# Kernel optimization log

Measured on AMD Instinct MI355X. Metric: run time of the kernel, lower is better.

Reference implementation:

```python
import jax, jax.numpy as jnp
import numpy as np

TSZ, BSZ, E, H = 1024, 8, 1024, 16


def setup_inputs() -> dict:
    key = jax.random.key(0)
    ks = jax.random.split(key, 7)
    s = 0.02
    return {
        "q": jax.random.normal(ks[0], (TSZ, BSZ, E), jnp.float32),
        "k": jax.random.normal(ks[1], (TSZ, BSZ, E), jnp.float32),
        "v": jax.random.normal(ks[2], (TSZ, BSZ, E), jnp.float32),
        "in_proj_weight": jax.random.normal(ks[3], (3 * E, E), jnp.float32) * s,
        "in_proj_bias": jax.random.normal(ks[4], (3 * E,), jnp.float32) * s,
        "out_proj_weight": jax.random.normal(ks[5], (E, E), jnp.float32) * s,
        "out_proj_bias": jax.random.normal(ks[6], (E,), jnp.float32) * s,
        "num_heads": H,
    }


def reference(q, k, v, in_proj_weight, in_proj_bias, out_proj_weight, out_proj_bias, num_heads):
    tsz, bsz, embed_dim = q.shape
    head_dim = embed_dim // num_heads
    scaling = float(head_dim) ** -0.5

    # in-projections (F.linear: x @ W.T + b), weight sliced into q/k/v chunks
    qp = q @ in_proj_weight[:embed_dim].T + in_proj_bias[:embed_dim]
    kp = k @ in_proj_weight[embed_dim:2 * embed_dim].T + in_proj_bias[embed_dim:2 * embed_dim]
    vp = v @ in_proj_weight[2 * embed_dim:].T + in_proj_bias[2 * embed_dim:]
    qp = qp * scaling

    # (tsz, bsz, E) -> (bsz*H, tsz, head_dim)
    def to_heads(x):
        return x.reshape(tsz, bsz * num_heads, head_dim).transpose(1, 0, 2)

    qh, kh, vh = to_heads(qp), to_heads(kp), to_heads(vp)

    # scaled dot-product attention (no mask, dropout p=0)
    scores = jnp.einsum('bqd,bkd->bqk', qh, kh)  # [bsz*H, tsz, tsz]
    weights = jax.nn.softmax(scores, axis=-1)
    attn = jnp.einsum('bqk,bkd->bqd', weights, vh)

    # back to (tsz, bsz, E), then out projection
    attn = attn.transpose(1, 0, 2).reshape(tsz, bsz, embed_dim)
    out = attn @ out_proj_weight.T + out_proj_bias
    return out
```

## Files before the change

### kernel.cpp

```cpp
#include <hip/hip_runtime.h>

typedef __bf16 bf16;
typedef __attribute__((ext_vector_type(8))) __bf16 v8bf;
typedef __attribute__((ext_vector_type(4))) __bf16 v4bf;
typedef __attribute__((ext_vector_type(4))) float f32x4;

static_assert(sizeof(v8bf) == 16, "v8bf must be 16B");

#define MFMA16(a, b, c) __builtin_amdgcn_mfma_f32_16x16x32_bf16((a), (b), (c), 0, 0, 0)

__device__ __forceinline__ void async_lds16(const bf16* g, bf16* l) {
  __builtin_amdgcn_global_load_lds(
      (__attribute__((address_space(1))) void*)(g),
      (__attribute__((address_space(3))) void*)(l), 16, 0, 0);
}

__global__ __launch_bounds__(256) void cvt_kernel(
    const float* __restrict__ q, const float* __restrict__ k,
    const float* __restrict__ v, const float* __restrict__ wi,
    const float* __restrict__ wo, bf16* __restrict__ xq, bf16* __restrict__ xk,
    bf16* __restrict__ xv, bf16* __restrict__ Wb, bf16* __restrict__ Wob) {
  int idx = blockIdx.x * 256 + threadIdx.x;
  const float4* src;
  v4bf* dst;
  int off;
  if (idx < 2097152)      { src = (const float4*)q;  dst = (v4bf*)xq;  off = idx; }
  else if (idx < 4194304) { src = (const float4*)k;  dst = (v4bf*)xk;  off = idx - 2097152; }
  else if (idx < 6291456) { src = (const float4*)v;  dst = (v4bf*)xv;  off = idx - 4194304; }
  else if (idx < 7077888) { src = (const float4*)wi; dst = (v4bf*)Wb;  off = idx - 6291456; }
  else                    { src = (const float4*)wo; dst = (v4bf*)Wob; off = idx - 7077888; }
  float4 f = src[off];
  v4bf b;
  b[0] = (bf16)f.x; b[1] = (bf16)f.y; b[2] = (bf16)f.z; b[3] = (bf16)f.w;
  dst[off] = b;
}

#define STAGE_A(S, MH, KO)                                                    \
  do {                                                                        \
    async_lds16(Xa + (size_t)((MH) * 128 + srA0) * 1024 + (KO) + skA0,        \
                &Asm[S][MH][ldst]);                                           \
    async_lds16(Xa + (size_t)((MH) * 128 + srA1) * 1024 + (KO) + skA1,        \
                &Asm[S][MH][4096 + ldst]);                                    \
  } while (0)

#define STAGE_B(S, NH, KO)                                                    \
  async_lds16(Wbase + (size_t)((NH) * 64 + srB) * 1024 + (KO) + skB,          \
              &Bsm[S][NH][ldst])

#define KTILE(S, NS, KN)                                                      \
  do {                                                                        \
    v8bf af0[4][2], af1[4][2], bf0[2], bf1[2];                                \
                                                            \
    _Pragma("unroll") for (int rt = 0; rt < 4; ++rt) {                        \
      af0[rt][0] = *(const v8bf*)&Asm[S][0][aro + rt * 1024 + rslot0];        \
      af0[rt][1] = *(const v8bf*)&Asm[S][0][aro + rt * 1024 + rslot1];        \
    }                                                                         \
    bf0[0] = *(const v8bf*)&Bsm[S][0][bro + rslot0];                          \
    bf0[1] = *(const v8bf*)&Bsm[S][0][bro + rslot1];                          \
    STAGE_A(NS, 0, KN);                                                       \
    asm volatile("s_waitcnt vmcnt(2)" ::: "memory");                          \
    __builtin_amdgcn_s_barrier();                                             \
    __builtin_amdgcn_s_setprio(1);                                            \
    _Pragma("unroll") for (int rt = 0; rt < 4; ++rt) {                        \
      acc[rt][0] = MFMA16(af0[rt][0], bf0[0], acc[rt][0]);                    \
      acc[rt][0] = MFMA16(af0[rt][1], bf0[1], acc[rt][0]);                    \
    }                                                                         \
    __builtin_amdgcn_s_setprio(0);                                            \
                                                            \
    _Pragma("unroll") for (int rt = 0; rt < 4; ++rt) {                        \
      af1[rt][0] = *(const v8bf*)&Asm[S][1][aro + rt * 1024 + rslot0];        \
      af1[rt][1] = *(const v8bf*)&Asm[S][1][aro + rt * 1024 + rslot1];        \
    }                                                                         \
    bf1[0] = *(const v8bf*)&Bsm[S][1][bro + rslot0];                          \
    bf1[1] = *(const v8bf*)&Bsm[S][1][bro + rslot1];                          \
    STAGE_B(NS, 0, KN);                                                       \
    __builtin_amdgcn_s_barrier();                                             \
    __builtin_amdgcn_s_setprio(1);                                            \
    _Pragma("unroll") for (int rt = 0; rt < 4; ++rt) {                        \
      acc[4 + rt][1] = MFMA16(af1[rt][0], bf1[0], acc[4 + rt][1]);            \
      acc[4 + rt][1] = MFMA16(af1[rt][1], bf1[1], acc[4 + rt][1]);            \
    }                                                                         \
    __builtin_amdgcn_s_setprio(0);                                            \
                                                            \
    STAGE_A(NS, 1, KN);                                                       \
    __builtin_amdgcn_s_barrier();                                             \
    __builtin_amdgcn_s_setprio(1);                                            \
    _Pragma("unroll") for (int rt = 0; rt < 4; ++rt) {                        \
      acc[4 + rt][0] = MFMA16(af1[rt][0], bf0[0], acc[4 + rt][0]);            \
      acc[4 + rt][0] = MFMA16(af1[rt][1], bf0[1], acc[4 + rt][0]);            \
    }                                                                         \
    __builtin_amdgcn_s_setprio(0);                                            \
                                                            \
    STAGE_B(NS, 1, KN);                                                       \
    asm volatile("s_waitcnt vmcnt(3)" ::: "memory");                          \
    __builtin_amdgcn_s_barrier();                                             \
    __builtin_amdgcn_s_setprio(1);                                            \
    _Pragma("unroll") for (int rt = 0; rt < 4; ++rt) {                        \
      acc[rt][1] = MFMA16(af0[rt][0], bf1[0], acc[rt][1]);                    \
      acc[rt][1] = MFMA16(af0[rt][1], bf1[1], acc[rt][1]);                    \
    }                                                                         \
    __builtin_amdgcn_s_setprio(0);                                            \
  } while (0)

#define GEMM_PRELUDE()                                                        \
  const int tid = threadIdx.x;                                                \
  const int w = tid >> 6, l = tid & 63, quad = l >> 4, lr = l & 15;           \
  const int wmg = w >> 2, wng = w & 3;                                        \
  const int srA0 = tid >> 3;                                                  \
  const int skA0 = (((tid & 7) ^ (srA0 & 7)) * 8);                            \
  const int srA1 = (512 + tid) >> 3;                                          \
  const int skA1 = (((tid & 7) ^ (srA1 & 7)) * 8);                            \
  const int srB = tid >> 3;                                                   \
  const int skB = (((tid & 7) ^ (srB & 7)) * 8);                              \
  const int ldst = (tid & ~63) * 8;                                           \
  const int aro = (wmg * 64 + lr) * 64;                                       \
  const int bro = (wng * 16 + lr) * 64;                                       \
  const int rslot0 = ((quad) ^ (lr & 7)) * 8;                                 \
  const int rslot1 = ((4 + quad) ^ (lr & 7)) * 8;                             \
  f32x4 acc[8][2] = {};                                                       \
        \
  STAGE_A(0, 0, 0);                                                           \
  STAGE_B(0, 0, 0);                                                           \
  STAGE_A(0, 1, 0);                                                           \
  STAGE_B(0, 1, 0);                                                           \
  asm volatile("s_waitcnt vmcnt(3)" ::: "memory");                            \
  __builtin_amdgcn_s_barrier();                                               \
  _Pragma("unroll 1") for (int t = 0; t < 16; t += 2) {                       \
    const int k1 = (t + 1) * 64;                                              \
    const int k2 = (t == 14) ? 0 : (t + 2) * 64;  \
    KTILE(0, 1, k1);                                                          \
    KTILE(1, 0, k2);                                                          \
  }                                                                           \
  asm volatile("s_waitcnt vmcnt(0)" ::: "memory");

__global__ __launch_bounds__(512, 2) void qkv_proj_kernel(
    const bf16* __restrict__ xq, const bf16* __restrict__ xk,
    const bf16* __restrict__ xv, const bf16* __restrict__ Wb,
    const float* __restrict__ bias, bf16* __restrict__ oq,
    bf16* __restrict__ ok, bf16* __restrict__ ov) {
  __shared__ bf16 Asm[2][2][128 * 64];
  __shared__ bf16 Bsm[2][2][64 * 64];
  const int L = blockIdx.x;
  const int r = L & 7, rest = L >> 3;
  const int m0 = (r * 4 + (rest & 3)) * 256;
  const int n0 = ((rest >> 2) & 7) * 128;
  const int c = rest >> 5;
  const bf16* X = (c == 0) ? xq : (c == 1) ? xk : xv;
  bf16* outp = (c == 0) ? oq : (c == 1) ? ok : ov;
  const bf16* Xa = X + (size_t)m0 * 1024;
  const bf16* Wbase = Wb + ((size_t)(c * 1024 + n0)) * 1024;

  GEMM_PRELUDE();

  const float scale = (c == 0) ? 0.125f : 1.0f;
#pragma unroll
  for (int mh = 0; mh < 2; ++mh)
#pragma unroll
    for (int rt = 0; rt < 4; ++rt)
#pragma unroll
      for (int nh = 0; nh < 2; ++nh) {
        const int n = n0 + nh * 64 + wng * 16 + lr;
        const float bn = bias[c * 1024 + n];
        const int hh = n >> 6, d = n & 63;
#pragma unroll
        for (int j = 0; j < 4; ++j) {
          const int m = m0 + mh * 128 + wmg * 64 + rt * 16 + quad * 4 + j;
          const int t_ = m >> 3, b = m & 7;
          outp[((size_t)((b * 16 + hh) * 1024 + t_)) * 64 + d] =
              (bf16)((acc[mh * 4 + rt][nh][j] + bn) * scale);
        }
      }
}

__global__ __launch_bounds__(256) void transpose_v_kernel(const bf16* __restrict__ vin,
                                                          bf16* __restrict__ vout) {
  __shared__ bf16 tile[64][72];
  const int bh = blockIdx.x;
  const int t0 = blockIdx.y * 64;
  const int tid = threadIdx.x;
  const int row = tid >> 2, cg = (tid & 3) * 16;
  const bf16* src = vin + ((size_t)bh * 1024 + t0 + row) * 64 + cg;
#pragma unroll
  for (int i = 0; i < 2; ++i) {
    v8bf x = *(const v8bf*)(src + i * 8);
#pragma unroll
    for (int jj = 0; jj < 8; ++jj) tile[row][cg + i * 8 + jj] = x[jj];
  }
  __syncthreads();
  const int d = tid >> 2, tg = (tid & 3) * 16;
  bf16* dst = vout + ((size_t)bh * 64 + d) * 1024 + t0 + tg;
  v8bf o0, o1;
#pragma unroll
  for (int i = 0; i < 8; ++i) o0[i] = tile[tg + i][d];
#pragma unroll
  for (int i = 0; i < 8; ++i) o1[i] = tile[tg + 8 + i][d];
  *(v8bf*)dst = o0;
  *(v8bf*)(dst + 8) = o1;
}

#define KSTR 72
#define VSTR 136

__global__ __launch_bounds__(256, 2) void attn_kernel(const bf16* __restrict__ qh,
                                                      const bf16* __restrict__ kh,
                                                      const bf16* __restrict__ vT,
                                                      bf16* __restrict__ attn_out) {
  __shared__ bf16 Ksm[128 * KSTR];
  __shared__ bf16 Vsm[64 * VSTR];
  __shared__ bf16 Psm[128 * VSTR];
  const int L = blockIdx.x;
  const int bh = (L & 7) * 16 + ((L >> 3) & 15);
  const int t0 = (L >> 7) * 128;
  const int tid = threadIdx.x;
  const int w = tid >> 6, l = tid & 63, quad = l >> 4, lr = l & 15;
  const int qr0 = t0 + w * 32;

  const bf16* khead = kh + (size_t)bh * 1024 * 64;
  const bf16* vhead = vT + (size_t)bh * 64 * 1024;

  const size_t qbase = ((size_t)bh * 1024 + qr0 + lr) * 64 + quad * 8;
  const v8bf bq00 = *(const v8bf*)(qh + qbase);
  const v8bf bq01 = *(const v8bf*)(qh + qbase + 32);
  const v8bf bq10 = *(const v8bf*)(qh + qbase + 1024);
  const v8bf bq11 = *(const v8bf*)(qh + qbase + 1024 + 32);

  const int krow = tid >> 1, kd = (tid & 1) * 32;
  const int vrow = tid >> 2, vk = (tid & 3) * 32;
  const bf16* kg = khead + (size_t)krow * 64 + kd;
  const bf16* vg = vhead + (size_t)vrow * 1024 + vk;
  bf16* Kw = &Ksm[krow * KSTR + kd];
  bf16* Vw = &Vsm[vrow * VSTR + vk];
  bf16* Pw = &Psm[w * 32 * VSTR];

  v8bf kst[4], vst[4];
#pragma unroll
  for (int i = 0; i < 4; ++i) kst[i] = *(const v8bf*)(kg + i * 8);
#pragma unroll
  for (int i = 0; i < 4; ++i) vst[i] = *(const v8bf*)(vg + i * 8);

  float rsum0 = 0.0f, rsum1 = 0.0f;
  f32x4 oacc0[4] = {}, oacc1[4] = {};

  for (int c = 0; c < 8; ++c) {
    __syncthreads();
#pragma unroll
    for (int i = 0; i < 4; ++i) *(v8bf*)(Kw + i * 8) = kst[i];
#pragma unroll
    for (int i = 0; i < 4; ++i) *(v8bf*)(Vw + i * 8) = vst[i];
    __syncthreads();
    if (c < 7) {
      const bf16* kg2 = kg + (size_t)(c + 1) * 128 * 64;
      const bf16* vg2 = vg + (c + 1) * 128;
#pragma unroll
      for (int i = 0; i < 4; ++i) kst[i] = *(const v8bf*)(kg2 + i * 8);
#pragma unroll
      for (int i = 0; i < 4; ++i) vst[i] = *(const v8bf*)(vg2 + i * 8);
    }

#pragma unroll
    for (int kt = 0; kt < 8; ++kt) {
      const v8bf ak0 = *(const v8bf*)&Ksm[(kt * 16 + lr) * KSTR + quad * 8];
      const v8bf ak1 = *(const v8bf*)&Ksm[(kt * 16 + lr) * KSTR + 32 + quad * 8];
      f32x4 a = {};
      a = MFMA16(ak0, bq00, a);
      a = MFMA16(ak1, bq01, a);
      f32x4 b = {};
      b = MFMA16(ak0, bq10, b);
      b = MFMA16(ak1, bq11, b);
      v4bf pb0, pb1;
#pragma unroll
      for (int j = 0; j < 4; ++j) {
        const float p0 = __expf(a[j]);
        const float p1 = __expf(b[j]);
        rsum0 += p0;
        rsum1 += p1;
        pb0[j] = (bf16)p0;
        pb1[j] = (bf16)p1;
      }
      *(v4bf*)(Pw + lr * VSTR + kt * 16 + quad * 4) = pb0;
      *(v4bf*)(Pw + (16 + lr) * VSTR + kt * 16 + quad * 4) = pb1;
    }

#pragma unroll
    for (int ks = 0; ks < 4; ++ks) {
      const v8bf pa0 = *(const v8bf*)(Pw + lr * VSTR + ks * 32 + quad * 8);
      const v8bf pa1 = *(const v8bf*)(Pw + (16 + lr) * VSTR + ks * 32 + quad * 8);
#pragma unroll
      for (int dt = 0; dt < 4; ++dt) {
        const v8bf vb = *(const v8bf*)&Vsm[(dt * 16 + lr) * VSTR + ks * 32 + quad * 8];
        oacc0[dt] = MFMA16(pa0, vb, oacc0[dt]);
        oacc1[dt] = MFMA16(pa1, vb, oacc1[dt]);
      }
    }
  }

  rsum0 += __shfl_xor(rsum0, 16);
  rsum0 += __shfl_xor(rsum0, 32);
  rsum1 += __shfl_xor(rsum1, 16);
  rsum1 += __shfl_xor(rsum1, 32);
  const float inv0 = 1.0f / rsum0;
  const float inv1 = 1.0f / rsum1;
  const int b = bh >> 4, h = bh & 15;
#pragma unroll
  for (int j = 0; j < 4; ++j) {
    const float i0 = __shfl(inv0, quad * 4 + j);
    const float i1 = __shfl(inv1, quad * 4 + j);
    const int t0j = qr0 + quad * 4 + j;
#pragma unroll
    for (int dt = 0; dt < 4; ++dt) {
      attn_out[((size_t)(t0j * 8 + b)) * 1024 + h * 64 + dt * 16 + lr] =
          (bf16)(oacc0[dt][j] * i0);
      attn_out[((size_t)((t0j + 16) * 8 + b)) * 1024 + h * 64 + dt * 16 + lr] =
          (bf16)(oacc1[dt][j] * i1);
    }
  }
}

__global__ __launch_bounds__(512, 2) void out_proj_kernel(const bf16* __restrict__ A,
                                                          const bf16* __restrict__ Wob,
                                                          const float* __restrict__ bias,
                                                          float* __restrict__ out) {
  __shared__ bf16 Asm[2][2][128 * 64];
  __shared__ bf16 Bsm[2][2][64 * 64];
  const int L = blockIdx.x;
  const int r = L & 7, rest = L >> 3;
  const int m0 = (r * 4 + (rest & 3)) * 256;
  const int n0 = (rest >> 2) * 128;
  const bf16* Xa = A + (size_t)m0 * 1024;
  const bf16* Wbase = Wob + (size_t)n0 * 1024;

  GEMM_PRELUDE();

#pragma unroll
  for (int mh = 0; mh < 2; ++mh)
#pragma unroll
    for (int rt = 0; rt < 4; ++rt)
#pragma unroll
      for (int nh = 0; nh < 2; ++nh) {
        const int n = n0 + nh * 64 + wng * 16 + lr;
        const float bn = bias[n];
#pragma unroll
        for (int j = 0; j < 4; ++j) {
          const int m = m0 + mh * 128 + wmg * 64 + rt * 16 + quad * 4 + j;
          out[(size_t)m * 1024 + n] = acc[mh * 4 + rt][nh][j] + bn;
        }
      }
}

extern "C" void kernel_launch(void* const* d_in, const int* in_sizes, int n_in,
                              void* d_out, int out_size, void* d_ws, size_t ws_size,
                              hipStream_t stream) {
  const float* q  = (const float*)d_in[0];
  const float* k  = (const float*)d_in[1];
  const float* v  = (const float*)d_in[2];
  const float* wi = (const float*)d_in[3];
  const float* bi = (const float*)d_in[4];
  const float* wo = (const float*)d_in[5];
  const float* bo = (const float*)d_in[6];
  float* out = (float*)d_out;
  char* ws = (char*)d_ws;
  const size_t MB = (size_t)1 << 20;
  bf16* Wb     = (bf16*)(ws + 0 * MB);
  bf16* Wob    = (bf16*)(ws + 6 * MB);
  bf16* wsq    = (bf16*)(ws + 8 * MB);
  bf16* wsk    = (bf16*)(ws + 24 * MB);
  bf16* wsv    = (bf16*)(ws + 40 * MB);
  bf16* xv     = (bf16*)(ws + 56 * MB);
  bf16* wsvT   = (bf16*)(ws + 56 * MB);
  bf16* xq     = (bf16*)d_out;
  bf16* xk     = (bf16*)((char*)d_out + 16 * MB);
  bf16* wsattn = wsv;

  cvt_kernel<<<dim3(28672), dim3(256), 0, stream>>>(q, k, v, wi, wo, xq, xk, xv, Wb, Wob);
  qkv_proj_kernel<<<dim3(768), dim3(512), 0, stream>>>(xq, xk, xv, Wb, bi, wsq, wsk, wsv);
  transpose_v_kernel<<<dim3(128, 16), dim3(256), 0, stream>>>(wsv, wsvT);
  attn_kernel<<<dim3(1024), dim3(256), 0, stream>>>(wsq, wsk, wsvT, wsattn);
  out_proj_kernel<<<dim3(512 / 2), dim3(512), 0, stream>>>(wsattn, Wob, bo, out);
}
```

Measured before the change: 296.3 us.

## Triple-buffer GEMM K-tiles and remap warps to 64x64 output subtiles

The shared GEMM prelude used by the QKV and output projections moves from a double-buffered split half-tile pipeline to a three-stage ring of full 256x64 A and 128x64 B tiles, prefetching two K-tiles ahead. Each of the 8 warps now owns a 64x64 output block (4x4 MFMA tiles) instead of 128x32, which lets A and B fragments be reused across more MFMAs per LDS read. The aim is to hide global-load latency better and cut LDS traffic per MFMA. In exchange, LDS use rises to 144KB per block, which could limit occupancy to one block per CU despite launch bounds requesting two.

```diff
diff --git a/kernel.cpp b/kernel.cpp
--- a/kernel.cpp
+++ b/kernel.cpp
@@ -35,69 +35,72 @@
   dst[off] = b;
 }
 
-#define STAGE_A(S, MH, KO)                                                    \
+#define A_TSZ (256 * 64)
+#define B_TSZ (128 * 64)
+
+#define STAGE6(SBUF, KO)                                                      \
   do {                                                                        \
-    async_lds16(Xa + (size_t)((MH) * 128 + srA0) * 1024 + (KO) + skA0,        \
-                &Asm[S][MH][ldst]);                                           \
-    async_lds16(Xa + (size_t)((MH) * 128 + srA1) * 1024 + (KO) + skA1,        \
-                &Asm[S][MH][4096 + ldst]);                                    \
+    bf16* Ad = Asmb + (SBUF) * A_TSZ + ldst;                                  \
+    bf16* Bd = Bsmb + (SBUF) * B_TSZ + ldst;                                  \
+    _Pragma("unroll") for (int i = 0; i < 4; ++i)                             \
+        async_lds16(Xa + (size_t)sAr[i] * 1024 + (KO) + sAk[i],               \
+                    Ad + i * 4096);                                           \
+    _Pragma("unroll") for (int i = 0; i < 2; ++i)                             \
+        async_lds16(Wbase + (size_t)sBr[i] * 1024 + (KO) + sBk[i],            \
+                    Bd + i * 4096);                                           \
   } while (0)
 
-#define STAGE_B(S, NH, KO)                                                    \
-  async_lds16(Wbase + (size_t)((NH) * 64 + srB) * 1024 + (KO) + skB,          \
-              &Bsm[S][NH][ldst])
-
-#define KTILE(S, NS, KN)                                                      \
+#define KTILE_BODY(CUR, STAGE_STMT, WAIT_STMT)                                \
   do {                                                                        \
-    v8bf af0[4][2], af1[4][2], bf0[2], bf1[2];                                \
-                                                            \
-    _Pragma("unroll") for (int rt = 0; rt < 4; ++rt) {                        \
-      af0[rt][0] = *(const v8bf*)&Asm[S][0][aro + rt * 1024 + rslot0];        \
-      af0[rt][1] = *(const v8bf*)&Asm[S][0][aro + rt * 1024 + rslot1];        \
-    }                                                                         \
-    bf0[0] = *(const v8bf*)&Bsm[S][0][bro + rslot0];                          \
-    bf0[1] = *(const v8bf*)&Bsm[S][0][bro + rslot1];                          \
-    STAGE_A(NS, 0, KN);                                                       \
-    asm volatile("s_waitcnt vmcnt(2)" ::: "memory");                          \
+    const bf16* Ab = Asmb + (CUR) * A_TSZ;                                    \
+    const bf16* Bb = Bsmb + (CUR) * B_TSZ;                                    \
+    v8bf af0[4], af1[4], bf0[4], bf1[4];                                      \
+                                      \
+    _Pragma("unroll") for (int rt = 0; rt < 4; ++rt)                          \
+        af0[rt] = *(const v8bf*)&Ab[aro + rt * 1024 + rslot0];                \
+    bf0[0] = *(const v8bf*)&Bb[bro + rslot0];                                 \
+    bf0[1] = *(const v8bf*)&Bb[bro + 1024 + rslot0];                          \
     __builtin_amdgcn_s_barrier();                                             \
     __builtin_amdgcn_s_setprio(1);                                            \
     _Pragma("unroll") for (int rt = 0; rt < 4; ++rt) {                        \
-      acc[rt][0] = MFMA16(af0[rt][0], bf0[0], acc[rt][0]);                    \
-      acc[rt][0] = MFMA16(af0[rt][1], bf0[1], acc[rt][0]);                    \
+      acc[rt][0] = MFMA16(af0[rt], bf0[0], acc[rt][0]);                       \
+      acc[rt][1] = MFMA16(af0[rt], bf0[1], acc[rt][1]);                       \
     }                                                                         \
     __builtin_amdgcn_s_setprio(0);                                            \
-                                                            \
-    _Pragma("unroll") for (int rt = 0; rt < 4; ++rt) {                        \
-      af1[rt][0] = *(const v8bf*)&Asm[S][1][aro + rt * 1024 + rslot0];        \
-      af1[rt][1] = *(const v8bf*)&Asm[S][1][aro + rt * 1024 + rslot1];        \
-    }                                                                         \
-    bf1[0] = *(const v8bf*)&Bsm[S][1][bro + rslot0];                          \
-    bf1[1] = *(const v8bf*)&Bsm[S][1][bro + rslot1];                          \
-    STAGE_B(NS, 0, KN);                                                       \
+                           \
+    bf0[2] = *(const v8bf*)&Bb[bro + 2048 + rslot0];                          \
+    bf0[3] = *(const v8bf*)&Bb[bro + 3072 + rslot0];                          \
+    af1[0] = *(const v8bf*)&Ab[aro + rslot1];                                 \
+    af1[1] = *(const v8bf*)&Ab[aro + 1024 + rslot1];                          \
+    STAGE_STMT                                                                \
     __builtin_amdgcn_s_barrier();                                             \
     __builtin_amdgcn_s_setprio(1);                                            \
     _Pragma("unroll") for (int rt = 0; rt < 4; ++rt) {                        \
-      acc[4 + rt][1] = MFMA16(af1[rt][0], bf1[0], acc[4 + rt][1]);            \
-      acc[4 + rt][1] = MFMA16(af1[rt][1], bf1[1], acc[4 + rt][1]);            \
+      acc[rt][2] = MFMA16(af0[rt], bf0[2], acc[rt][2]);                       \
+      acc[rt][3] = MFMA16(af0[rt], bf0[3], acc[rt][3]);                       \
     }                                                                         \
     __builtin_amdgcn_s_setprio(0);                                            \
-                                                            \
-    STAGE_A(NS, 1, KN);                                                       \
+                                      \
+    af1[2] = *(const v8bf*)&Ab[aro + 2048 + rslot1];                          \
+    af1[3] = *(const v8bf*)&Ab[aro + 3072 + rslot1];                          \
+    bf1[0] = *(const v8bf*)&Bb[bro + rslot1];                                 \
+    bf1[1] = *(const v8bf*)&Bb[bro + 1024 + rslot1];                          \
     __builtin_amdgcn_s_barrier();                                             \
     __builtin_amdgcn_s_setprio(1);                                            \
     _Pragma("unroll") for (int rt = 0; rt < 4; ++rt) {                        \
-      acc[4 + rt][0] = MFMA16(af1[rt][0], bf0[0], acc[4 + rt][0]);            \
-      acc[4 + rt][0] = MFMA16(af1[rt][1], bf0[1], acc[4 + rt][0]);            \
+      acc[rt][0] = MFMA16(af1[rt], bf1[0], acc[rt][0]);                       \
+      acc[rt][1] = MFMA16(af1[rt], bf1[1], acc[rt][1]);                       \
     }                                                                         \
     __builtin_amdgcn_s_setprio(0);                                            \
-                                                            \
-    STAGE_B(NS, 1, KN);                                                       \
-    asm volatile("s_waitcnt vmcnt(3)" ::: "memory");                          \
+                                          \
+    bf1[2] = *(const v8bf*)&Bb[bro + 2048 + rslot1];                          \
+    bf1[3] = *(const v8bf*)&Bb[bro + 3072 + rslot1];                          \
+    WAIT_STMT                                                                 \
     __builtin_amdgcn_s_barrier();                                             \
     __builtin_amdgcn_s_setprio(1);                                            \
     _Pragma("unroll") for (int rt = 0; rt < 4; ++rt) {                        \
-      acc[rt][1] = MFMA16(af0[rt][0], bf1[0], acc[rt][1]);                    \
-      acc[rt][1] = MFMA16(af0[rt][1], bf1[1], acc[rt][1]);                    \
+      acc[rt][2] = MFMA16(af1[rt], bf1[2], acc[rt][2]);                       \
+      acc[rt][3] = MFMA16(af1[rt], bf1[3], acc[rt][3]);                       \
     }                                                                         \
     __builtin_amdgcn_s_setprio(0);                                            \
   } while (0)
@@ -105,41 +108,50 @@
 #define GEMM_PRELUDE()                                                        \
   const int tid = threadIdx.x;                                                \
   const int w = tid >> 6, l = tid & 63, quad = l >> 4, lr = l & 15;           \
-  const int wmg = w >> 2, wng = w & 3;                                        \
-  const int srA0 = tid >> 3;                                                  \
-  const int skA0 = (((tid & 7) ^ (srA0 & 7)) * 8);                            \
-  const int srA1 = (512 + tid) >> 3;                                          \
-  const int skA1 = (((tid & 7) ^ (srA1 & 7)) * 8);                            \
-  const int srB = tid >> 3;                                                   \
-  const int skB = (((tid & 7) ^ (srB & 7)) * 8);                              \
+  const int wmg = w >> 1, wng = w & 1;                                        \
+  int sAr[4], sAk[4];                                                         \
+  _Pragma("unroll") for (int i = 0; i < 4; ++i) {                             \
+    sAr[i] = (i * 512 + tid) >> 3;                                            \
+    sAk[i] = ((tid & 7) ^ (sAr[i] & 7)) * 8;                                  \
+  }                                                                           \
+  int sBr[2], sBk[2];                                                         \
+  _Pragma("unroll") for (int i = 0; i < 2; ++i) {                             \
+    sBr[i] = (i * 512 + tid) >> 3;                                            \
+    sBk[i] = ((tid & 7) ^ (sBr[i] & 7)) * 8;                                  \
+  }                                                                           \
   const int ldst = (tid & ~63) * 8;                                           \
   const int aro = (wmg * 64 + lr) * 64;                                       \
-  const int bro = (wng * 16 + lr) * 64;                                       \
+  const int bro = (wng * 64 + lr) * 64;                                       \
   const int rslot0 = ((quad) ^ (lr & 7)) * 8;                                 \
   const int rslot1 = ((4 + quad) ^ (lr & 7)) * 8;                             \
-  f32x4 acc[8][2] = {};                                                       \
-        \
-  STAGE_A(0, 0, 0);                                                           \
-  STAGE_B(0, 0, 0);                                                           \
-  STAGE_A(0, 1, 0);                                                           \
-  STAGE_B(0, 1, 0);                                                           \
-  asm volatile("s_waitcnt vmcnt(3)" ::: "memory");                            \
+  f32x4 acc[4][4] = {};                                                       \
+       \
+  STAGE6(0, 0);                                                               \
+  STAGE6(1, 64);                                                              \
+  asm volatile("s_waitcnt vmcnt(6)" ::: "memory");                            \
   __builtin_amdgcn_s_barrier();                                               \
-  _Pragma("unroll 1") for (int t = 0; t < 16; t += 2) {                       \
-    const int k1 = (t + 1) * 64;                                              \
-    const int k2 = (t == 14) ? 0 : (t + 2) * 64;  \
-    KTILE(0, 1, k1);                                                          \
-    KTILE(1, 0, k2);                                                          \
+  int cur = 0;                                                                \
+  _Pragma("unroll 1") for (int t = 0; t < 14; ++t) {                          \
+    const int nxt = (cur >= 1) ? cur - 1 : 2;                  \
+    KTILE_BODY(cur, STAGE6(nxt, (t + 2) * 64);,                               \
+               asm volatile("s_waitcnt vmcnt(6)" ::: "memory"););             \
+    cur = (cur == 2) ? 0 : cur + 1;                                           \
   }                                                                           \
-  asm volatile("s_waitcnt vmcnt(0)" ::: "memory");
+            \
+  KTILE_BODY(cur, , asm volatile("s_waitcnt vmcnt(0)" ::: "memory"););        \
+  cur = (cur == 2) ? 0 : cur + 1;                                             \
+                                               \
+  KTILE_BODY(cur, , )
 
 __global__ __launch_bounds__(512, 2) void qkv_proj_kernel(
     const bf16* __restrict__ xq, const bf16* __restrict__ xk,
     const bf16* __restrict__ xv, const bf16* __restrict__ Wb,
     const float* __restrict__ bias, bf16* __restrict__ oq,
     bf16* __restrict__ ok, bf16* __restrict__ ov) {
-  __shared__ bf16 Asm[2][2][128 * 64];
-  __shared__ bf16 Bsm[2][2][64 * 64];
+  __shared__ bf16 Asm[3][A_TSZ];
+  __shared__ bf16 Bsm[3][B_TSZ];
+  bf16* Asmb = &Asm[0][0];
+  bf16* Bsmb = &Bsm[0][0];
   const int L = blockIdx.x;
   const int r = L & 7, rest = L >> 3;
   const int m0 = (r * 4 + (rest & 3)) * 256;
@@ -154,22 +166,20 @@
 
   const float scale = (c == 0) ? 0.125f : 1.0f;
 #pragma unroll
-  for (int mh = 0; mh < 2; ++mh)
-#pragma unroll
-    for (int rt = 0; rt < 4; ++rt)
-#pragma unroll
-      for (int nh = 0; nh < 2; ++nh) {
-        const int n = n0 + nh * 64 + wng * 16 + lr;
-        const float bn = bias[c * 1024 + n];
-        const int hh = n >> 6, d = n & 63;
-#pragma unroll
-        for (int j = 0; j < 4; ++j) {
-          const int m = m0 + mh * 128 + wmg * 64 + rt * 16 + quad * 4 + j;
-          const int t_ = m >> 3, b = m & 7;
-          outp[((size_t)((b * 16 + hh) * 1024 + t_)) * 64 + d] =
-              (bf16)((acc[mh * 4 + rt][nh][j] + bn) * scale);
-        }
+  for (int rt = 0; rt < 4; ++rt)
+#pragma unroll
+    for (int ct = 0; ct < 4; ++ct) {
+      const int n = n0 + wng * 64 + ct * 16 + lr;
+      const float bn = bias[c * 1024 + n];
+      const int hh = n >> 6, d = n & 63;
+#pragma unroll
+      for (int j = 0; j < 4; ++j) {
+        const int m = m0 + wmg * 64 + rt * 16 + quad * 4 + j;
+        const int t_ = m >> 3, b = m & 7;
+        outp[((size_t)((b * 16 + hh) * 1024 + t_)) * 64 + d] =
+            (bf16)((acc[rt][ct][j] + bn) * scale);
       }
+    }
 }
 
 __global__ __launch_bounds__(256) void transpose_v_kernel(const bf16* __restrict__ vin,
@@ -320,8 +330,10 @@
                                                           const bf16* __restrict__ Wob,
                                                           const float* __restrict__ bias,
                                                           float* __restrict__ out) {
-  __shared__ bf16 Asm[2][2][128 * 64];
-  __shared__ bf16 Bsm[2][2][64 * 64];
+  __shared__ bf16 Asm[3][A_TSZ];
+  __shared__ bf16 Bsm[3][B_TSZ];
+  bf16* Asmb = &Asm[0][0];
+  bf16* Bsmb = &Bsm[0][0];
   const int L = blockIdx.x;
   const int r = L & 7, rest = L >> 3;
   const int m0 = (r * 4 + (rest & 3)) * 256;
@@ -332,19 +344,17 @@
   GEMM_PRELUDE();
 
 #pragma unroll
-  for (int mh = 0; mh < 2; ++mh)
-#pragma unroll
-    for (int rt = 0; rt < 4; ++rt)
-#pragma unroll
-      for (int nh = 0; nh < 2; ++nh) {
-        const int n = n0 + nh * 64 + wng * 16 + lr;
-        const float bn = bias[n];
-#pragma unroll
-        for (int j = 0; j < 4; ++j) {
-          const int m = m0 + mh * 128 + wmg * 64 + rt * 16 + quad * 4 + j;
-          out[(size_t)m * 1024 + n] = acc[mh * 4 + rt][nh][j] + bn;
-        }
+  for (int rt = 0; rt < 4; ++rt)
+#pragma unroll
+    for (int ct = 0; ct < 4; ++ct) {
+      const int n = n0 + wng * 64 + ct * 16 + lr;
+      const float bn = bias[n];
+#pragma unroll
+      for (int j = 0; j < 4; ++j) {
+        const int m = m0 + wmg * 64 + rt * 16 + quad * 4 + j;
+        out[(size_t)m * 1024 + n] = acc[rt][ct][j] + bn;
       }
+    }
 }
 
 extern "C" void kernel_launch(void* const* d_in, const int* in_sizes, int n_in,
@@ -375,5 +385,5 @@
   qkv_proj_kernel<<<dim3(768), dim3(512), 0, stream>>>(xq, xk, xv, Wb, bi, wsq, wsk, wsv);
   transpose_v_kernel<<<dim3(128, 16), dim3(256), 0, stream>>>(wsv, wsvT);
   attn_kernel<<<dim3(1024), dim3(256), 0, stream>>>(wsq, wsk, wsvT, wsattn);
-  out_proj_kernel<<<dim3(512 / 2), dim3(512), 0, stream>>>(wsattn, Wob, bo, out);
-}
+  out_proj_kernel<<<dim3(256), dim3(512), 0, stream>>>(wsattn, Wob, bo, out);
+}
```

After: 300.8 us. No clear change (+1.5%).

## Rewrite projection GEMMs with 256x256 tiles and 32x32x16 MFMA

Applied to the files above, without the earlier changes.

Replaces the 256x128 tile, 512-thread GEMM core used by the QKV and output projections with a 256x256 tile, 256-thread design. Each wave computes a 128x128 sub-tile using 32x32x16 bf16 MFMAs, with a new XOR swizzle and simple double buffering. Larger per-wave tiles raise register reuse and cut LDS reads per FLOP. In exchange, the grids shrink to 384 and 128 blocks at one block per CU, so occupancy and the number of blocks per CU drop. The previous fine-grained interleaving of staging and compute is gone, replaced by a full vmcnt(0) wait per tile.

```diff
diff --git a/kernel.cpp b/kernel.cpp
--- a/kernel.cpp
+++ b/kernel.cpp
@@ -4,10 +4,12 @@
 typedef __attribute__((ext_vector_type(8))) __bf16 v8bf;
 typedef __attribute__((ext_vector_type(4))) __bf16 v4bf;
 typedef __attribute__((ext_vector_type(4))) float f32x4;
+typedef __attribute__((ext_vector_type(16))) float f32x16;
 
 static_assert(sizeof(v8bf) == 16, "v8bf must be 16B");
 
 #define MFMA16(a, b, c) __builtin_amdgcn_mfma_f32_16x16x32_bf16((a), (b), (c), 0, 0, 0)
+#define MFMA32(a, b, c) __builtin_amdgcn_mfma_f32_32x32x16_bf16((a), (b), (c), 0, 0, 0)
 
 __device__ __forceinline__ void async_lds16(const bf16* g, bf16* l) {
   __builtin_amdgcn_global_load_lds(
@@ -35,141 +37,123 @@
   dst[off] = b;
 }
 
-#define STAGE_A(S, MH, KO)                                                    \
+#define TSZ (256 * 64)
+
+#define STAGE32(BUF, KO)                                                      \
   do {                                                                        \
-    async_lds16(Xa + (size_t)((MH) * 128 + srA0) * 1024 + (KO) + skA0,        \
-                &Asm[S][MH][ldst]);                                           \
-    async_lds16(Xa + (size_t)((MH) * 128 + srA1) * 1024 + (KO) + skA1,        \
-                &Asm[S][MH][4096 + ldst]);                                    \
+    bf16* Ad = Asmb + (BUF) * TSZ + wdst;                                     \
+    bf16* Bd = Bsmb + (BUF) * TSZ + wdst;                                     \
+    _Pragma("unroll") for (int i = 0; i < 8; ++i)                             \
+        async_lds16(Xa + (size_t)sOff[i] + (KO), Ad + i * 2048);              \
+    _Pragma("unroll") for (int i = 0; i < 8; ++i)                             \
+        async_lds16(Wbase + (size_t)sOff[i] + (KO), Bd + i * 2048);           \
   } while (0)
 
-#define STAGE_B(S, NH, KO)                                                    \
-  async_lds16(Wbase + (size_t)((NH) * 64 + srB) * 1024 + (KO) + skB,          \
-              &Bsm[S][NH][ldst])
-
-#define KTILE(S, NS, KN)                                                      \
+#define LOADA(BUF, MH)                                                        \
+  _Pragma("unroll") for (int ks = 0; ks < 4; ++ks) {                          \
+    aR[0][ks] = *(const v8bf*)&Asmb[(BUF) * TSZ + aBase + (MH) * 4096 +       \
+                                    ((ks * 16) ^ plA8)];                      \
+    aR[1][ks] = *(const v8bf*)&Asmb[(BUF) * TSZ + aBase + (MH) * 4096 +       \
+                                    2048 + ((ks * 16) ^ 32 ^ plA8)];          \
+  }
+
+#define LOADB(BUF, NH)                                                        \
+  _Pragma("unroll") for (int ks = 0; ks < 4; ++ks) {                          \
+    bR[NH][0][ks] = *(const v8bf*)&Bsmb[(BUF) * TSZ + bBase + (NH) * 4096 +   \
+                                        ((ks * 16) ^ plA8)];                  \
+    bR[NH][1][ks] = *(const v8bf*)&Bsmb[(BUF) * TSZ + bBase + (NH) * 4096 +   \
+                                        2048 + ((ks * 16) ^ 32 ^ plA8)];      \
+  }
+
+#define MFMAQ(MH, NH)                                                         \
+  _Pragma("unroll") for (int ks = 0; ks < 4; ++ks) {                          \
+    acc[(MH)*2+0][(NH)*2+0] =                                                 \
+        MFMA32(aR[0][ks], bR[NH][0][ks], acc[(MH)*2+0][(NH)*2+0]);            \
+    acc[(MH)*2+0][(NH)*2+1] =                                                 \
+        MFMA32(aR[0][ks], bR[NH][1][ks], acc[(MH)*2+0][(NH)*2+1]);            \
+    acc[(MH)*2+1][(NH)*2+0] =                                                 \
+        MFMA32(aR[1][ks], bR[NH][0][ks], acc[(MH)*2+1][(NH)*2+0]);            \
+    acc[(MH)*2+1][(NH)*2+1] =                                                 \
+        MFMA32(aR[1][ks], bR[NH][1][ks], acc[(MH)*2+1][(NH)*2+1]);            \
+  }
+
+#define TILE32(BUF, STAGE_STMT)                                               \
   do {                                                                        \
-    v8bf af0[4][2], af1[4][2], bf0[2], bf1[2];                                \
-                                                            \
-    _Pragma("unroll") for (int rt = 0; rt < 4; ++rt) {                        \
-      af0[rt][0] = *(const v8bf*)&Asm[S][0][aro + rt * 1024 + rslot0];        \
-      af0[rt][1] = *(const v8bf*)&Asm[S][0][aro + rt * 1024 + rslot1];        \
-    }                                                                         \
-    bf0[0] = *(const v8bf*)&Bsm[S][0][bro + rslot0];                          \
-    bf0[1] = *(const v8bf*)&Bsm[S][0][bro + rslot1];                          \
-    STAGE_A(NS, 0, KN);                                                       \
-    asm volatile("s_waitcnt vmcnt(2)" ::: "memory");                          \
+    STAGE_STMT;                                                               \
+    LOADA(BUF, 0)                                                             \
+    LOADB(BUF, 0)                                                             \
+    MFMAQ(0, 0)                                                               \
+    LOADB(BUF, 1)                                                             \
+    MFMAQ(0, 1)                                                               \
+    LOADA(BUF, 1)                                                             \
+    MFMAQ(1, 1)                                                               \
+    MFMAQ(1, 0)                                                               \
+    asm volatile("s_waitcnt vmcnt(0)" ::: "memory");                          \
     __builtin_amdgcn_s_barrier();                                             \
-    __builtin_amdgcn_s_setprio(1);                                            \
-    _Pragma("unroll") for (int rt = 0; rt < 4; ++rt) {                        \
-      acc[rt][0] = MFMA16(af0[rt][0], bf0[0], acc[rt][0]);                    \
-      acc[rt][0] = MFMA16(af0[rt][1], bf0[1], acc[rt][0]);                    \
-    }                                                                         \
-    __builtin_amdgcn_s_setprio(0);                                            \
-                                                            \
-    _Pragma("unroll") for (int rt = 0; rt < 4; ++rt) {                        \
-      af1[rt][0] = *(const v8bf*)&Asm[S][1][aro + rt * 1024 + rslot0];        \
-      af1[rt][1] = *(const v8bf*)&Asm[S][1][aro + rt * 1024 + rslot1];        \
-    }                                                                         \
-    bf1[0] = *(const v8bf*)&Bsm[S][1][bro + rslot0];                          \
-    bf1[1] = *(const v8bf*)&Bsm[S][1][bro + rslot1];                          \
-    STAGE_B(NS, 0, KN);                                                       \
-    __builtin_amdgcn_s_barrier();                                             \
-    __builtin_amdgcn_s_setprio(1);                                            \
-    _Pragma("unroll") for (int rt = 0; rt < 4; ++rt) {                        \
-      acc[4 + rt][1] = MFMA16(af1[rt][0], bf1[0], acc[4 + rt][1]);            \
-      acc[4 + rt][1] = MFMA16(af1[rt][1], bf1[1], acc[4 + rt][1]);            \
-    }                                                                         \
-    __builtin_amdgcn_s_setprio(0);                                            \
-                                                            \
-    STAGE_A(NS, 1, KN);                                                       \
-    __builtin_amdgcn_s_barrier();                                             \
-    __builtin_amdgcn_s_setprio(1);                                            \
-    _Pragma("unroll") for (int rt = 0; rt < 4; ++rt) {                        \
-      acc[4 + rt][0] = MFMA16(af1[rt][0], bf0[0], acc[4 + rt][0]);            \
-      acc[4 + rt][0] = MFMA16(af1[rt][1], bf0[1], acc[4 + rt][0]);            \
-    }                                                                         \
-    __builtin_amdgcn_s_setprio(0);                                            \
-                                                            \
-    STAGE_B(NS, 1, KN);                                                       \
-    asm volatile("s_waitcnt vmcnt(3)" ::: "memory");                          \
-    __builtin_amdgcn_s_barrier();                                             \
-    __builtin_amdgcn_s_setprio(1);                                            \
-    _Pragma("unroll") for (int rt = 0; rt < 4; ++rt) {                        \
-      acc[rt][1] = MFMA16(af0[rt][0], bf1[0], acc[rt][1]);                    \
-      acc[rt][1] = MFMA16(af0[rt][1], bf1[1], acc[rt][1]);                    \
-    }                                                                         \
-    __builtin_amdgcn_s_setprio(0);                                            \
   } while (0)
 
-#define GEMM_PRELUDE()                                                        \
+#define GEMM32_PRELUDE()                                                      \
   const int tid = threadIdx.x;                                                \
-  const int w = tid >> 6, l = tid & 63, quad = l >> 4, lr = l & 15;           \
-  const int wmg = w >> 2, wng = w & 3;                                        \
-  const int srA0 = tid >> 3;                                                  \
-  const int skA0 = (((tid & 7) ^ (srA0 & 7)) * 8);                            \
-  const int srA1 = (512 + tid) >> 3;                                          \
-  const int skA1 = (((tid & 7) ^ (srA1 & 7)) * 8);                            \
-  const int srB = tid >> 3;                                                   \
-  const int skB = (((tid & 7) ^ (srB & 7)) * 8);                              \
-  const int ldst = (tid & ~63) * 8;                                           \
-  const int aro = (wmg * 64 + lr) * 64;                                       \
-  const int bro = (wng * 16 + lr) * 64;                                       \
-  const int rslot0 = ((quad) ^ (lr & 7)) * 8;                                 \
-  const int rslot1 = ((4 + quad) ^ (lr & 7)) * 8;                             \
-  f32x4 acc[8][2] = {};                                                       \
-        \
-  STAGE_A(0, 0, 0);                                                           \
-  STAGE_B(0, 0, 0);                                                           \
-  STAGE_A(0, 1, 0);                                                           \
-  STAGE_B(0, 1, 0);                                                           \
-  asm volatile("s_waitcnt vmcnt(3)" ::: "memory");                            \
+  const int w = tid >> 6, l = tid & 63;                                       \
+  const int wm = w >> 1, wn = w & 1;                                          \
+  const int c31 = l & 31, kh = l >> 5;                                        \
+  const int plA8 = ((kh ^ c31 ^ (c31 >> 3)) & 7) * 8;                         \
+  const int aBase = (wm * 128 + c31) * 64;                                    \
+  const int bBase = (wn * 128 + c31) * 64;                                    \
+  const int wdst = (tid & ~63) * 8;                                           \
+  int sOff[8];                                                                \
+  _Pragma("unroll") for (int i = 0; i < 8; ++i) {                             \
+    const int ch = i * 256 + tid;                                             \
+    const int rw = ch >> 3;                                                   \
+    sOff[i] = rw * 1024 + (((ch & 7) ^ ((rw ^ (rw >> 3)) & 7)) * 8);          \
+  }                                                                           \
+  v8bf aR[2][4], bR[2][2][4];                                                 \
+  f32x16 acc[4][4] = {};                                                      \
+  STAGE32(0, 0);                                                              \
+  asm volatile("s_waitcnt vmcnt(0)" ::: "memory");                            \
   __builtin_amdgcn_s_barrier();                                               \
   _Pragma("unroll 1") for (int t = 0; t < 16; t += 2) {                       \
-    const int k1 = (t + 1) * 64;                                              \
-    const int k2 = (t == 14) ? 0 : (t + 2) * 64;  \
-    KTILE(0, 1, k1);                                                          \
-    KTILE(1, 0, k2);                                                          \
-  }                                                                           \
-  asm volatile("s_waitcnt vmcnt(0)" ::: "memory");
-
-__global__ __launch_bounds__(512, 2) void qkv_proj_kernel(
+    TILE32(0, STAGE32(1, (t + 1) * 64));                                      \
+    TILE32(1, if (t < 14) STAGE32(0, (t + 2) * 64));                          \
+  }
+
+__global__ __launch_bounds__(256, 1) void qkv_proj_kernel(
     const bf16* __restrict__ xq, const bf16* __restrict__ xk,
     const bf16* __restrict__ xv, const bf16* __restrict__ Wb,
     const float* __restrict__ bias, bf16* __restrict__ oq,
     bf16* __restrict__ ok, bf16* __restrict__ ov) {
-  __shared__ bf16 Asm[2][2][128 * 64];
-  __shared__ bf16 Bsm[2][2][64 * 64];
+  __shared__ bf16 Asm2[2][TSZ];
+  __shared__ bf16 Bsm2[2][TSZ];
+  bf16* Asmb = &Asm2[0][0];
+  bf16* Bsmb = &Bsm2[0][0];
   const int L = blockIdx.x;
-  const int r = L & 7, rest = L >> 3;
-  const int m0 = (r * 4 + (rest & 3)) * 256;
-  const int n0 = ((rest >> 2) & 7) * 128;
-  const int c = rest >> 5;
+  const int g = L >> 5;
+  const int c = g >> 2;
+  const int n0 = (g & 3) * 256;
+  const int m0 = (L & 31) * 256;
   const bf16* X = (c == 0) ? xq : (c == 1) ? xk : xv;
   bf16* outp = (c == 0) ? oq : (c == 1) ? ok : ov;
   const bf16* Xa = X + (size_t)m0 * 1024;
   const bf16* Wbase = Wb + ((size_t)(c * 1024 + n0)) * 1024;
 
-  GEMM_PRELUDE();
+  GEMM32_PRELUDE();
 
   const float scale = (c == 0) ? 0.125f : 1.0f;
 #pragma unroll
-  for (int mh = 0; mh < 2; ++mh)
-#pragma unroll
-    for (int rt = 0; rt < 4; ++rt)
-#pragma unroll
-      for (int nh = 0; nh < 2; ++nh) {
-        const int n = n0 + nh * 64 + wng * 16 + lr;
-        const float bn = bias[c * 1024 + n];
-        const int hh = n >> 6, d = n & 63;
-#pragma unroll
-        for (int j = 0; j < 4; ++j) {
-          const int m = m0 + mh * 128 + wmg * 64 + rt * 16 + quad * 4 + j;
-          const int t_ = m >> 3, b = m & 7;
-          outp[((size_t)((b * 16 + hh) * 1024 + t_)) * 64 + d] =
-              (bf16)((acc[mh * 4 + rt][nh][j] + bn) * scale);
-        }
+  for (int mf = 0; mf < 4; ++mf)
+#pragma unroll
+    for (int nf = 0; nf < 4; ++nf) {
+      const int n = n0 + wn * 128 + nf * 32 + c31;
+      const float bn = bias[c * 1024 + n];
+      const int hh = n >> 6, d = n & 63;
+#pragma unroll
+      for (int r = 0; r < 16; ++r) {
+        const int m = m0 + wm * 128 + mf * 32 + (r & 3) + ((r >> 2) * 8) + kh * 4;
+        const int t_ = m >> 3, b = m & 7;
+        outp[((size_t)((b * 16 + hh) * 1024 + t_)) * 64 + d] =
+            (bf16)((acc[mf][nf][r] + bn) * scale);
       }
+    }
 }
 
 __global__ __launch_bounds__(256) void transpose_v_kernel(const bf16* __restrict__ vin,
@@ -316,35 +300,34 @@
   }
 }
 
-__global__ __launch_bounds__(512, 2) void out_proj_kernel(const bf16* __restrict__ A,
+__global__ __launch_bounds__(256, 1) void out_proj_kernel(const bf16* __restrict__ A,
                                                           const bf16* __restrict__ Wob,
                                                           const float* __restrict__ bias,
                                                           float* __restrict__ out) {
-  __shared__ bf16 Asm[2][2][128 * 64];
-  __shared__ bf16 Bsm[2][2][64 * 64];
+  __shared__ bf16 Asm2[2][TSZ];
+  __shared__ bf16 Bsm2[2][TSZ];
+  bf16* Asmb = &Asm2[0][0];
+  bf16* Bsmb = &Bsm2[0][0];
   const int L = blockIdx.x;
-  const int r = L & 7, rest = L >> 3;
-  const int m0 = (r * 4 + (rest & 3)) * 256;
-  const int n0 = (rest >> 2) * 128;
+  const int n0 = (L >> 5) * 256;
+  const int m0 = (L & 31) * 256;
   const bf16* Xa = A + (size_t)m0 * 1024;
   const bf16* Wbase = Wob + (size_t)n0 * 1024;
 
-  GEMM_PRELUDE();
-
-#pragma unroll
-  for (int mh = 0; mh < 2; ++mh)
-#pragma unroll
-    for (int rt = 0; rt < 4; ++rt)
-#pragma unroll
-      for (int nh = 0; nh < 2; ++nh) {
-        const int n = n0 + nh * 64 + wng * 16 + lr;
-        const float bn = bias[n];
-#pragma unroll
-        for (int j = 0; j < 4; ++j) {
-          const int m = m0 + mh * 128 + wmg * 64 + rt * 16 + quad * 4 + j;
-          out[(size_t)m * 1024 + n] = acc[mh * 4 + rt][nh][j] + bn;
-        }
+  GEMM32_PRELUDE();
+
+#pragma unroll
+  for (int mf = 0; mf < 4; ++mf)
+#pragma unroll
+    for (int nf = 0; nf < 4; ++nf) {
+      const int n = n0 + wn * 128 + nf * 32 + c31;
+      const float bn = bias[n];
+#pragma unroll
+      for (int r = 0; r < 16; ++r) {
+        const int m = m0 + wm * 128 + mf * 32 + (r & 3) + ((r >> 2) * 8) + kh * 4;
+        out[(size_t)m * 1024 + n] = acc[mf][nf][r] + bn;
       }
+    }
 }
 
 extern "C" void kernel_launch(void* const* d_in, const int* in_sizes, int n_in,
@@ -372,8 +355,8 @@
   bf16* wsattn = wsv;
 
   cvt_kernel<<<dim3(28672), dim3(256), 0, stream>>>(q, k, v, wi, wo, xq, xk, xv, Wb, Wob);
-  qkv_proj_kernel<<<dim3(768), dim3(512), 0, stream>>>(xq, xk, xv, Wb, bi, wsq, wsk, wsv);
+  qkv_proj_kernel<<<dim3(384), dim3(256), 0, stream>>>(xq, xk, xv, Wb, bi, wsq, wsk, wsv);
   transpose_v_kernel<<<dim3(128, 16), dim3(256), 0, stream>>>(wsv, wsvT);
   attn_kernel<<<dim3(1024), dim3(256), 0, stream>>>(wsq, wsk, wsvT, wsattn);
-  out_proj_kernel<<<dim3(512 / 2), dim3(512), 0, stream>>>(wsattn, Wob, bo, out);
-}
+  out_proj_kernel<<<dim3(128), dim3(256), 0, stream>>>(wsattn, Wob, bo, out);
+}
```

Result: slower. 436.6 us (+47.4%).
